# Kernel tuning notes

Hardware: AMD Instinct MI355X
Metric: run time of the kernel (lower is better)

## Reference

```python
import jax, jax.numpy as jnp
import numpy as np

OFFSET = 3  # windows 3,5,7


def _maxpool_same(x, k):
    # MaxPool2d(kernel=k, stride=1, padding=(k-1)//2); torch pads with -inf
    p = (k - 1) // 2
    return jax.lax.reduce_window(
        x, -jnp.inf, jax.lax.max,
        window_dimensions=(1, 1, k, k),
        window_strides=(1, 1, 1, 1),
        padding=((0, 0), (0, 0), (p, p), (p, p)))


def setup_inputs() -> dict:
    key = jax.random.key(0)
    # strictly positive so log10 is finite
    x = jax.random.uniform(key, (8, 64, 256, 256), dtype=jnp.float32,
                           minval=1e-3, maxval=1.0)
    return {"x": x}


def reference(x) -> jnp.ndarray:
    B, C, H, W = x.shape
    windows = jnp.array([2.0 * i + 1.0 for i in range(1, OFFSET + 1)],
                        dtype=x.dtype)  # [3,5,7]
    xs = jnp.log10(windows / (H * W))
    xc = xs - xs.mean()
    # Closed-form OLS slope weights: inv(X X^T) X reduces analytically to
    # w_i = (x_i - xbar) / sum_j (x_j - xbar)^2 for the slope row.
    w = xc / jnp.sum(xc * xc)                  # [OFFSET]
    # slope = sum_i w_i * log10(maxpool_{k_i}(x)), computed without stacking
    holder = jnp.zeros_like(x)
    for i in range(OFFSET):
        k = 2 * (i + 1) + 1
        holder = holder + w[i] * jnp.log10(_maxpool_same(x, k))
    return holder  # (B, C, H, W)
```

## Files before the change

kernel.cpp:

```cpp
#include <hip/hip_runtime.h>
#include <cmath>


#define IMG_H 256
#define IMG_W 256
#define SROWS 64
#define LEAD  8

typedef float vf4 __attribute__((ext_vector_type(4)));

__device__ __forceinline__ vf4 aload(const float* base, uint32_t voff) {
  vf4 r;
  asm volatile("global_load_dwordx4 %0, %1, %2"
               : "=v"(r) : "v"(voff), "s"(base) : "memory");
  return r;
}

__device__ __forceinline__ void wait_all11(vf4& a, vf4& b, vf4& c, vf4& d,
                                           vf4& e, vf4& f, vf4& g, vf4& h,
                                           vf4& i, vf4& j, vf4& k) {
  asm volatile("s_waitcnt vmcnt(0)"
               : "+v"(a), "+v"(b), "+v"(c), "+v"(d), "+v"(e), "+v"(f),
                 "+v"(g), "+v"(h), "+v"(i), "+v"(j), "+v"(k) :: "memory");
}

__device__ __forceinline__ void wait10_w7(vf4& a, vf4& b, vf4& c, vf4& d,
                                          vf4& e, vf4& f, vf4& g) {
  asm volatile("s_waitcnt vmcnt(10)"
               : "+v"(a), "+v"(b), "+v"(c), "+v"(d), "+v"(e), "+v"(f),
                 "+v"(g) :: "memory");
}

__device__ __forceinline__ float dpp_left(float v) {
  return __int_as_float(
      __builtin_amdgcn_update_dpp(0, __float_as_int(v), 0x138, 0xF, 0xF, true));
}
__device__ __forceinline__ float dpp_right(float v) {
  return __int_as_float(
      __builtin_amdgcn_update_dpp(0, __float_as_int(v), 0x130, 0xF, 0xF, true));
}

__device__ __forceinline__ vf4 vmax(vf4 a, vf4 b) {
  vf4 r;
  r.x = fmaxf(a.x, b.x); r.y = fmaxf(a.y, b.y);
  r.z = fmaxf(a.z, b.z); r.w = fmaxf(a.w, b.w);
  return r;
}

struct PS { float p1, p2, p3, s1, s2, s3, f; };

__device__ __forceinline__ PS make_ps(vf4 a) {
  PS r;
  r.p1 = a.x;
  r.p2 = fmaxf(a.x, a.y);
  r.p3 = fmaxf(r.p2, a.z);
  r.s1 = a.w;
  r.s2 = fmaxf(a.z, a.w);
  r.s3 = fmaxf(a.y, r.s2);
  r.f  = fmaxf(r.p2, r.s2);
  return r;
}

__device__ __forceinline__ vf4 row_out(vf4 wm3, vf4 wm2, vf4 wm1, vf4 wc,
                                       vf4 wp1, vf4 wp2, vf4 wp3,
                                       float w3, float w5, float w7) {
  vf4 v1 = vmax(vmax(wm1, wc), wp1);
  vf4 v2 = vmax(v1, vmax(wm2, wp2));
  vf4 v3 = vmax(v2, vmax(wm3, wp3));

  PS a1 = make_ps(v1), a2 = make_ps(v2), a3 = make_ps(v3);

  float L1s1 = dpp_left(a1.s1);
  float L2s1 = dpp_left(a2.s1);
  float L2s2 = dpp_left(a2.s2);
  float L3s1 = dpp_left(a3.s1);
  float L3s2 = dpp_left(a3.s2);
  float L3s3 = dpp_left(a3.s3);

  float R1p1 = dpp_right(a1.p1);
  float R2p1 = dpp_right(a2.p1);
  float R2p2 = dpp_right(a2.p2);
  float R3p1 = dpp_right(a3.p1);
  float R3p2 = dpp_right(a3.p2);
  float R3p3 = dpp_right(a3.p3);

  float m3_0 = fmaxf(L1s1, a1.p2);
  float m3_1 = a1.p3;
  float m3_2 = a1.s3;
  float m3_3 = fmaxf(a1.s2, R1p1);

  float m5_0 = fmaxf(L2s2, a2.p3);
  float m5_1 = fmaxf(L2s1, a2.f);
  float m5_2 = fmaxf(a2.f, R2p1);
  float m5_3 = fmaxf(a2.s3, R2p2);

  float m7_0 = fmaxf(L3s3, a3.f);
  float m7_1 = fmaxf(fmaxf(L3s2, a3.f), R3p1);
  float m7_2 = fmaxf(fmaxf(L3s1, a3.f), R3p2);
  float m7_3 = fmaxf(a3.f, R3p3);

  vf4 o;
  o.x = fmaf(w7, __log2f(m7_0), fmaf(w5, __log2f(m5_0), w3 * __log2f(m3_0)));
  o.y = fmaf(w7, __log2f(m7_1), fmaf(w5, __log2f(m5_1), w3 * __log2f(m3_1)));
  o.z = fmaf(w7, __log2f(m7_2), fmaf(w5, __log2f(m5_2), w3 * __log2f(m3_2)));
  o.w = fmaf(w7, __log2f(m7_3), fmaf(w5, __log2f(m5_3), w3 * __log2f(m3_3)));
  return o;
}

__global__ __launch_bounds__(64, 2) void holder_kernel(
    const float* __restrict__ x, float* __restrict__ out,
    float w3, float w5, float w7)
{
  const int lane  = threadIdx.x;
  const int img   = blockIdx.x;
  const int strip = blockIdx.y;
  const int r0    = strip * SROWS;

  const float* px = x + (size_t)img * (IMG_H * IMG_W);
  float*       po = out + (size_t)img * (IMG_H * IMG_W) + lane * 4;
  const uint32_t lo = (uint32_t)lane * 16u;

  const vf4 vzero = (vf4)0.0f;

  vf4 ring[16];

#pragma unroll
  for (int i = 0; i < 11; ++i) {
    int rr = r0 - 3 + i;
    int rc = rr < 0 ? 0 : rr;
    ring[(i + 13) & 15] = aload(px, (uint32_t)(rc * IMG_W * 4) + lo);
  }
  wait_all11(ring[13], ring[14], ring[15], ring[0], ring[1], ring[2],
             ring[3], ring[4], ring[5], ring[6], ring[7]);
  if (r0 == 0) { ring[13] = vzero; ring[14] = vzero; ring[15] = vzero; }

#pragma unroll 1
  for (int it = 0; it < SROWS / 16; ++it) {
    const int R = r0 + it * 16;
#pragma unroll
    for (int k = 0; k < 16; ++k) {
      {
        int rr = R + k + LEAD;
        int rc = rr > IMG_H - 1 ? IMG_H - 1 : rr;
        ring[(k + LEAD) & 15] = aload(px, (uint32_t)(rc * IMG_W * 4) + lo);
      }
      wait10_w7(ring[(k + 13) & 15], ring[(k + 14) & 15], ring[(k + 15) & 15],
                ring[k & 15], ring[(k + 1) & 15], ring[(k + 2) & 15],
                ring[(k + 3) & 15]);
      if (R + k + 3 > IMG_H - 1) ring[(k + 3) & 15] = vzero;
      vf4 o = row_out(ring[(k + 13) & 15], ring[(k + 14) & 15],
                      ring[(k + 15) & 15], ring[k & 15],
                      ring[(k + 1) & 15], ring[(k + 2) & 15],
                      ring[(k + 3) & 15], w3, w5, w7);
      *(vf4*)(po + (R + k) * IMG_W) = o;
    }
  }
}

extern "C" void kernel_launch(void* const* d_in, const int* in_sizes, int n_in,
                              void* d_out, int out_size, void* d_ws, size_t ws_size,
                              hipStream_t stream) {
  const float* x = (const float*)d_in[0];
  float* out = (float*)d_out;

  const int n_img = in_sizes[0] / (IMG_H * IMG_W);

  const double l0 = log10(3.0), l1 = log10(5.0), l2 = log10(7.0);
  const double m  = (l0 + l1 + l2) / 3.0;
  const double c0 = l0 - m, c1 = l1 - m, c2 = l2 - m;
  const double s  = c0 * c0 + c1 * c1 + c2 * c2;
  const double LG2 = 0.30102999566398119521;
  const float w3 = (float)(c0 / s * LG2);
  const float w5 = (float)(c1 / s * LG2);
  const float w7 = (float)(c2 / s * LG2);

  hipLaunchKernelGGL(holder_kernel, dim3(n_img, IMG_H / SROWS), dim3(64),
                     0, stream, x, out, w3, w5, w7);
}
```

Before: 235.4 us.

## Replace asm ring-buffer prefetch with compiler-scheduled sliding window, shorter strips

Drops the hand-written inline-asm loads and explicit vmcnt waits that kept an eight-row lead in a 16-entry register ring. It uses a plain seven-register sliding window, fully unrolled over 32 rows per wave, and leaves load scheduling to the compiler. Strips are halved, so the grid doubles, and launch bounds now allow four waves per EU to raise occupancy. The cost is more halo rows reloaded per strip, plus reliance on the compiler to hoist loads far enough ahead to hide memory latency.

```diff
diff --git a/kernel.cpp b/kernel.cpp
--- a/kernel.cpp
+++ b/kernel.cpp
@@ -4,32 +4,9 @@
 
 #define IMG_H 256
 #define IMG_W 256
-#define SROWS 64
-#define LEAD  8
+#define RPW   32
 
 typedef float vf4 __attribute__((ext_vector_type(4)));
-
-__device__ __forceinline__ vf4 aload(const float* base, uint32_t voff) {
-  vf4 r;
-  asm volatile("global_load_dwordx4 %0, %1, %2"
-               : "=v"(r) : "v"(voff), "s"(base) : "memory");
-  return r;
-}
-
-__device__ __forceinline__ void wait_all11(vf4& a, vf4& b, vf4& c, vf4& d,
-                                           vf4& e, vf4& f, vf4& g, vf4& h,
-                                           vf4& i, vf4& j, vf4& k) {
-  asm volatile("s_waitcnt vmcnt(0)"
-               : "+v"(a), "+v"(b), "+v"(c), "+v"(d), "+v"(e), "+v"(f),
-                 "+v"(g), "+v"(h), "+v"(i), "+v"(j), "+v"(k) :: "memory");
-}
-
-__device__ __forceinline__ void wait10_w7(vf4& a, vf4& b, vf4& c, vf4& d,
-                                          vf4& e, vf4& f, vf4& g) {
-  asm volatile("s_waitcnt vmcnt(10)"
-               : "+v"(a), "+v"(b), "+v"(c), "+v"(d), "+v"(e), "+v"(f),
-                 "+v"(g) :: "memory");
-}
 
 __device__ __forceinline__ float dpp_left(float v) {
   return __int_as_float(
@@ -40,7 +17,7 @@
       __builtin_amdgcn_update_dpp(0, __float_as_int(v), 0x130, 0xF, 0xF, true));
 }
 
-__device__ __forceinline__ vf4 vmax(vf4 a, vf4 b) {
+__device__ __forceinline__ vf4 vmax4(vf4 a, vf4 b) {
   vf4 r;
   r.x = fmaxf(a.x, b.x); r.y = fmaxf(a.y, b.y);
   r.z = fmaxf(a.z, b.z); r.w = fmaxf(a.w, b.w);
@@ -64,9 +41,9 @@
 __device__ __forceinline__ vf4 row_out(vf4 wm3, vf4 wm2, vf4 wm1, vf4 wc,
                                        vf4 wp1, vf4 wp2, vf4 wp3,
                                        float w3, float w5, float w7) {
-  vf4 v1 = vmax(vmax(wm1, wc), wp1);
-  vf4 v2 = vmax(v1, vmax(wm2, wp2));
-  vf4 v3 = vmax(v2, vmax(wm3, wp3));
+  vf4 v1 = vmax4(vmax4(wm1, wc), wp1);
+  vf4 v2 = vmax4(v1, vmax4(wm2, wp2));
+  vf4 v3 = vmax4(v2, vmax4(wm3, wp3));
 
   PS a1 = make_ps(v1), a2 = make_ps(v2), a3 = make_ps(v3);
 
@@ -107,53 +84,47 @@
   return o;
 }
 
-__global__ __launch_bounds__(64, 2) void holder_kernel(
+__global__ __launch_bounds__(64, 4) void holder_kernel(
     const float* __restrict__ x, float* __restrict__ out,
     float w3, float w5, float w7)
 {
   const int lane  = threadIdx.x;
   const int img   = blockIdx.x;
   const int strip = blockIdx.y;
-  const int r0    = strip * SROWS;
+  const int r0    = strip * RPW;
 
-  const float* px = x + (size_t)img * (IMG_H * IMG_W);
+  const float* px = x + (size_t)img * (IMG_H * IMG_W) + lane * 4;
   float*       po = out + (size_t)img * (IMG_H * IMG_W) + lane * 4;
-  const uint32_t lo = (uint32_t)lane * 16u;
 
   const vf4 vzero = (vf4)0.0f;
 
-  vf4 ring[16];
+  vf4 win0, win1, win2, win3, win4, win5, win6;
+  {
+    int rr, rc; vf4 t;
+    rr = r0 - 3; rc = rr < 0 ? 0 : rr;
+    t = *(const vf4*)(px + rc * IMG_W); win0 = rr < 0 ? vzero : t;
+    rr = r0 - 2; rc = rr < 0 ? 0 : rr;
+    t = *(const vf4*)(px + rc * IMG_W); win1 = rr < 0 ? vzero : t;
+    rr = r0 - 1; rc = rr < 0 ? 0 : rr;
+    t = *(const vf4*)(px + rc * IMG_W); win2 = rr < 0 ? vzero : t;
+    win3 = *(const vf4*)(px + (r0 + 0) * IMG_W);
+    win4 = *(const vf4*)(px + (r0 + 1) * IMG_W);
+    win5 = *(const vf4*)(px + (r0 + 2) * IMG_W);
+  }
 
 #pragma unroll
-  for (int i = 0; i < 11; ++i) {
-    int rr = r0 - 3 + i;
-    int rc = rr < 0 ? 0 : rr;
-    ring[(i + 13) & 15] = aload(px, (uint32_t)(rc * IMG_W * 4) + lo);
-  }
-  wait_all11(ring[13], ring[14], ring[15], ring[0], ring[1], ring[2],
-             ring[3], ring[4], ring[5], ring[6], ring[7]);
-  if (r0 == 0) { ring[13] = vzero; ring[14] = vzero; ring[15] = vzero; }
+  for (int k = 0; k < RPW; ++k) {
+    const int r  = r0 + k;
+    const int rn = r + 3;
+    const int rc = rn > IMG_H - 1 ? IMG_H - 1 : rn;
+    vf4 t = *(const vf4*)(px + rc * IMG_W);
+    win6 = rn > IMG_H - 1 ? vzero : t;
 
-#pragma unroll 1
-  for (int it = 0; it < SROWS / 16; ++it) {
-    const int R = r0 + it * 16;
-#pragma unroll
-    for (int k = 0; k < 16; ++k) {
-      {
-        int rr = R + k + LEAD;
-        int rc = rr > IMG_H - 1 ? IMG_H - 1 : rr;
-        ring[(k + LEAD) & 15] = aload(px, (uint32_t)(rc * IMG_W * 4) + lo);
-      }
-      wait10_w7(ring[(k + 13) & 15], ring[(k + 14) & 15], ring[(k + 15) & 15],
-                ring[k & 15], ring[(k + 1) & 15], ring[(k + 2) & 15],
-                ring[(k + 3) & 15]);
-      if (R + k + 3 > IMG_H - 1) ring[(k + 3) & 15] = vzero;
-      vf4 o = row_out(ring[(k + 13) & 15], ring[(k + 14) & 15],
-                      ring[(k + 15) & 15], ring[k & 15],
-                      ring[(k + 1) & 15], ring[(k + 2) & 15],
-                      ring[(k + 3) & 15], w3, w5, w7);
-      *(vf4*)(po + (R + k) * IMG_W) = o;
-    }
+    vf4 o = row_out(win0, win1, win2, win3, win4, win5, win6, w3, w5, w7);
+    *(vf4*)(po + r * IMG_W) = o;
+
+    win0 = win1; win1 = win2; win2 = win3;
+    win3 = win4; win4 = win5; win5 = win6;
   }
 }
 
@@ -174,6 +145,6 @@
   const float w5 = (float)(c1 / s * LG2);
   const float w7 = (float)(c2 / s * LG2);
 
-  hipLaunchKernelGGL(holder_kernel, dim3(n_img, IMG_H / SROWS), dim3(64),
+  hipLaunchKernelGGL(holder_kernel, dim3(n_img, IMG_H / RPW), dim3(64),
                      0, stream, x, out, w3, w5, w7);
 }
```

Result: no change. 237.9 us (+1.1%).
